# Performance work log

Measured on AMD Instinct MI355X. Metric: run time of the kernel, lower is better.

## Reference

```python
import jax, jax.numpy as jnp
import numpy as np

# arch config (matches init_kwargs)
T = 8
G = 16
D = 64
GG = G * G
THR = 0.5            # arch.object_threshold
Z_COS_MATCH_W = 5.0  # arch.z_cos_match_weight
ADJ_W = 1.0
PRES_W = 1.0
POOL_W = 1.0
OBJ_W = 10.0
FLOW_W = 1.0
FULL_OBJ = 200000.0  # arch.full_object_weight
FLOW_END = 100000.0  # arch.flow_cooling_end_step


def setup_inputs() -> dict:
    key = jax.random.key(0)
    k1, k2, k3 = jax.random.split(key, 3)
    B = 128
    return {
        "z_what": jax.random.normal(k1, (T * B, GG, D), dtype=jnp.float32),
        "z_pres_prob": jax.random.uniform(k2, (T * B, GG, 1), dtype=jnp.float32),
        "grid_flow": jax.random.uniform(k3, (T * B, GG, 1), dtype=jnp.float32),
        "global_step": 50000,
    }


def _maxpool3x3(x):
    # x: (N, C, G, G); torch MaxPool2d(3, stride=1, padding=1) pads with -inf
    return jax.lax.reduce_window(
        x, -jnp.inf, jax.lax.max,
        window_dimensions=(1, 1, 3, 3), window_strides=(1, 1, 1, 1),
        padding=[(0, 0), (0, 0), (1, 1), (1, 1)])


def reference(z_what, z_pres_prob, grid_flow, global_step):
    B = z_what.shape[0] // T
    zw = z_what.reshape(T, B, GG, D)
    zp = z_pres_prob.reshape(T, B, GG, 1)

    # ---- z_what_loss_grid_cell: adjacent squared deltas ----
    z_what_loss = jnp.sum((zw[1:] - zw[:-1]) ** 2)

    # ---- z_pres_loss_grid_cell ----
    sim = 1.0 - (zp[2:] - zp[:-2]) ** 2
    deltas = (zp[2:] - zp[1:-1]) ** 2 + (zp[:-2] - zp[1:-1]) ** 2
    z_pres_loss = jnp.sum(sim * deltas)

    # ---- z_what_consistency_pool (cosine_sim branch) ----
    w = jnp.abs(zw) * zp                                    # (T,B,GG,D)
    wi = w.transpose(0, 1, 3, 2).reshape(T * B, D, G, G)
    smoothed = _maxpool3x3(wi).reshape(T, B, D, GG).transpose(0, 1, 3, 2)
    dot = jnp.sum(smoothed[:-1] * w[1:], axis=-1)           # (T-1,B,GG)
    na = jnp.maximum(jnp.sqrt(jnp.sum(smoothed[:-1] ** 2, -1)), 1e-6)
    nb = jnp.maximum(jnp.sqrt(jnp.sum(w[1:] ** 2, -1)), 1e-6)
    cos_pool = dot / (na * nb)
    pw = zp[..., 0]
    pw = (pw[:-1] + pw[1:]) * 0.5                           # (T-1,B,GG)
    z_what_loss_pool = -jnp.sum(cos_pool * pw)

    # ---- z_what_consistency_objects (vectorized over objects) ----
    # For every active cell (t,b,i,j) at time t<T-1, compare its z_what (prior)
    # with z_what at t+1 over the 3x3 circular neighborhood, restricted to
    # neighbor cells whose z_pres > threshold. Loss per object:
    #   -z_cos_match_weight * max(sim) + sum(sim); skipped if no active neighbor.
    zpg = zp.reshape(T, B, G, G)
    zwg = zw.reshape(T, B, G, G, D)
    prior = zwg[:-1]                                        # (T-1,B,G,G,D)
    prior_n = jnp.maximum(jnp.sqrt(jnp.sum(prior ** 2, -1)), 1e-8)
    pres_prior = zpg[:-1] > THR                             # (T-1,B,G,G)
    sum_sim = jnp.zeros(prior.shape[:-1], dtype=prior.dtype)
    max_sim = jnp.full(prior.shape[:-1], -jnp.inf, dtype=prior.dtype)
    has_nb = jnp.zeros(prior.shape[:-1], dtype=bool)
    for di in (-1, 0, 1):
        for dj in (-1, 0, 1):
            nbw = jnp.roll(zwg[1:], (-di, -dj), axis=(2, 3))       # circular
            nbp = jnp.roll(zpg[1:], (-di, -dj), axis=(2, 3)) > THR
            dotn = jnp.sum(prior * nbw, axis=-1)
            nn = jnp.maximum(jnp.sqrt(jnp.sum(nbw ** 2, -1)), 1e-8)
            s = dotn / (prior_n * nn)
            sum_sim = sum_sim + jnp.where(nbp, s, 0.0)
            max_sim = jnp.maximum(max_sim, jnp.where(nbp, s, -jnp.inf))
            has_nb = has_nb | nbp
    valid = pres_prior & has_nb
    contrib = jnp.where(valid, -Z_COS_MATCH_W * max_sim + sum_sim, 0.0)
    z_what_loss_objects = jnp.sum(contrib)
    objects_detected = jnp.sum(pres_prior.astype(jnp.int32))

    # ---- compute_flow_loss ----
    zp_img = z_pres_prob.reshape(-1, 1, G, G)
    zp_max = _maxpool3x3(zp_img).reshape(-1, GG, 1)
    flow = grid_flow.reshape(-1, GG, 1)
    fmask = flow > 0.5
    flow_loss = jnp.sum(jnp.where(fmask, (zp_max - flow) ** 2, 0.0)) \
        + 100.0 * jnp.maximum(0.0, jnp.sum(zp_img) - jnp.sum(flow))

    # ---- total (Space base loss excluded; external submodule) ----
    scale_obj = min(1.0, float(global_step) / FULL_OBJ)
    scale_flow = max(0.0, 1.0 - float(global_step) / FLOW_END)
    loss = (z_what_loss * ADJ_W
            + z_pres_loss * PRES_W
            + z_what_loss_pool * POOL_W
            + z_what_loss_objects * scale_obj * OBJ_W
            + flow_loss * FLOW_W * scale_flow)
    return loss
```

## Files before the change

kernel.cpp:

```cpp
#include <hip/hip_runtime.h>
#include <math.h>

#define TT 8
#define BB 128
#define GG 256
#define DD 64
#define NCH 4
#define CF4 4
#define ST 5
#define NPAIR ((TT - 1) * BB)


__device__ inline float wred(float v) {
#pragma unroll
    for (int off = 32; off > 0; off >>= 1) v += __shfl_xor(v, off, 64);
    return v;
}
__device__ inline float dot4(float4 a, float4 b) {
    return a.x * b.x + a.y * b.y + a.z * b.z + a.w * b.w;
}
__device__ inline float4 fabs4(float4 a) {
    return make_float4(fabsf(a.x), fabsf(a.y), fabsf(a.z), fabsf(a.w));
}
__device__ inline float4 max4(float4 a, float4 b) {
    return make_float4(fmaxf(a.x, b.x), fmaxf(a.y, b.y), fmaxf(a.z, b.z), fmaxf(a.w, b.w));
}
__device__ inline float4 scale4(float4 a, float s) {
    return make_float4(a.x * s, a.y * s, a.z * s, a.w * s);
}
__device__ inline float4 sub4(float4 a, float4 b) {
    return make_float4(a.x - b.x, a.y - b.y, a.z - b.z, a.w - b.w);
}
__device__ inline float4 shfl4(float4 v, int src) {
    return make_float4(__shfl(v.x, src, 64), __shfl(v.y, src, 64),
                       __shfl(v.z, src, 64), __shfl(v.w, src, 64));
}

__global__ __launch_bounds__(256) void pair_kernel(const float* __restrict__ zw,
                                                   const float* __restrict__ zp,
                                                   const float* __restrict__ flow,
                                                   float* __restrict__ part) {
    const int pairIdx = blockIdx.x;
    const int t = pairIdx >> 7;
    const int b = pairIdx & (BB - 1);
    const int tid = threadIdx.x;
    const int gi = tid >> 4, gj = tid & 15;
    const int lane = tid & 63;

    __shared__ float4 shS[GG * ST];
    __shared__ float pA[GG], pB[GG], nB[GG];
    __shared__ float bred[8][4];

    const float4* gA = (const float4*)zw + (size_t)(t * BB + b) * 1024;
    const float4* gB = gA + (size_t)BB * 1024;

    const float pAc = zp[(size_t)(t * BB + b) * GG + tid];
    const float pBc = zp[(size_t)((t + 1) * BB + b) * GG + tid];
    pA[tid] = pAc;
    pB[tid] = pBc;

    int nbc[9];
    unsigned inbM = 0;
    {
        int m = 0;
#pragma unroll
        for (int di = -1; di <= 1; di++) {
#pragma unroll
            for (int dj = -1; dj <= 1; dj++) {
                nbc[m] = (((gi + di) & 15) << 4) | ((gj + dj) & 15);
                if (((unsigned)(gi + di) < 16u) && ((unsigned)(gj + dj) < 16u))
                    inbM |= (1u << m);
                m++;
            }
        }
    }
    __syncthreads();

    float zdiff = 0.f, sa = 0.f, sb = 0.f, poolDot = 0.f, poolN = 0.f;
    float dots[9] = {0.f, 0.f, 0.f, 0.f, 0.f, 0.f, 0.f, 0.f, 0.f};

#pragma unroll 1
    for (int c = 0; c < NCH; c++) {
        float4 aA[CF4], aB[CF4], rm[CF4];
#pragma unroll
        for (int q = 0; q < CF4; q++) {
            aA[q] = gA[tid * 16 + c * CF4 + q];
            aB[q] = gB[tid * 16 + c * CF4 + q];
        }
#pragma unroll
        for (int q = 0; q < CF4; q++) {
            float4 d = sub4(aB[q], aA[q]);
            zdiff += dot4(d, d);
            sa += dot4(aA[q], aA[q]);
            sb += dot4(aB[q], aB[q]);
            dots[4] += dot4(aA[q], aB[q]);
            float4 wa = scale4(fabs4(aA[q]), pAc);
            rm[q] = wa;
            float4 lft = shfl4(wa, lane - 1);
            if (gj > 0) rm[q] = max4(rm[q], lft);
            float4 rgt = shfl4(wa, lane + 1);
            if (gj < 15) rm[q] = max4(rm[q], rgt);
            shS[tid * ST + q] = aB[q];
        }
        __syncthreads();

#pragma unroll
        for (int k = 0; k < 9; k++) {
            if (k == 4) continue;
            int base = nbc[k] * ST;
#pragma unroll
            for (int q = 0; q < CF4; q++) dots[k] += dot4(aA[q], shS[base + q]);
        }
        __syncthreads();

#pragma unroll
        for (int q = 0; q < CF4; q++) shS[tid * ST + q] = rm[q];
        __syncthreads();

#pragma unroll
        for (int q = 0; q < CF4; q++) {
            float4 sm = rm[q];
            if (gi > 0) sm = max4(sm, shS[(tid - 16) * ST + q]);
            if (gi < 15) sm = max4(sm, shS[(tid + 16) * ST + q]);
            poolDot += dot4(sm, fabs4(aB[q]));
            poolN += dot4(sm, sm);
        }
        __syncthreads();
    }

    nB[tid] = sqrtf(sb);
    __syncthreads();

    float prior_n = fmaxf(sqrtf(sa), 1e-8f);
    float sum_sim = 0.f, max_sim = -1e30f;
    bool has = false;
#pragma unroll
    for (int k = 0; k < 9; k++) {
        float nn = fmaxf(nB[nbc[k]], 1e-8f);
        float s = dots[k] / (prior_n * nn);
        if (pB[nbc[k]] > 0.5f) {
            sum_sim += s;
            max_sim = fmaxf(max_sim, s);
            has = true;
        }
    }
    float obj = ((pAc > 0.5f) && has) ? (sum_sim - 5.0f * max_sim) : 0.f;

    float na_pool = fmaxf(sqrtf(poolN), 1e-6f);
    float nb_pool = fmaxf(pBc * sqrtf(sb), 1e-6f);
    float poolc = -(pBc * poolDot) / (na_pool * nb_pool) * 0.5f * (pAc + pBc);

    float mx = pAc;
#pragma unroll
    for (int k = 0; k < 9; k++)
        if (k != 4 && ((inbM >> k) & 1u)) mx = fmaxf(mx, pA[nbc[k]]);
    float f = flow[(size_t)(t * BB + b) * GG + tid];
    float fsq = 0.f;
    if (f > 0.5f) { float d = mx - f; fsq = d * d; }
    float szp = pAc, sflow = f;
    if (t == 6) {
        float mxB = pBc;
#pragma unroll
        for (int k = 0; k < 9; k++)
            if (k != 4 && ((inbM >> k) & 1u)) mxB = fmaxf(mxB, pB[nbc[k]]);
        float f7 = flow[(size_t)(7 * BB + b) * GG + tid];
        if (f7 > 0.5f) { float d = mxB - f7; fsq += d * d; }
        szp += pBc;
        sflow += f7;
    }

    float pres = 0.f;
    if (t <= 5) {
        float pC = zp[(size_t)((t + 2) * BB + b) * GG + tid];
        float s02 = pC - pAc;
        float sim = 1.f - s02 * s02;
        float d2 = pC - pBc, d0 = pAc - pBc;
        pres = sim * (d2 * d2 + d0 * d0);
    }

    float r[7] = {zdiff, pres, poolc, obj, fsq, szp, sflow};
    int w = tid >> 6;
#pragma unroll
    for (int j = 0; j < 7; j++) {
        float rv = wred(r[j]);
        if (lane == 0) bred[j][w] = rv;
    }
    __syncthreads();
    if (tid < 7)
        part[pairIdx * 8 + tid] = bred[tid][0] + bred[tid][1] + bred[tid][2] + bred[tid][3];
}

__global__ __launch_bounds__(256) void final_kernel(const float* __restrict__ part,
                                                    const int* __restrict__ gs,
                                                    float* __restrict__ out) {
    const int tid = threadIdx.x;
    __shared__ float bred[7][4];
    float c[7] = {0.f, 0.f, 0.f, 0.f, 0.f, 0.f, 0.f};
    for (int p = tid; p < NPAIR; p += 256) {
        const float* r = part + p * 8;
#pragma unroll
        for (int j = 0; j < 7; j++) c[j] += r[j];
    }
    int w = tid >> 6, lane = tid & 63;
#pragma unroll
    for (int j = 0; j < 7; j++) {
        float rv = wred(c[j]);
        if (lane == 0) bred[j][w] = rv;
    }
    __syncthreads();
    if (tid == 0) {
        float s[7];
#pragma unroll
        for (int j = 0; j < 7; j++) s[j] = bred[j][0] + bred[j][1] + bred[j][2] + bred[j][3];
        float step = (float)gs[0];
        float scale_obj = fminf(1.f, step / 200000.f);
        float scale_flow = fmaxf(0.f, 1.f - step / 100000.f);
        float flow_loss = s[4] + 100.f * fmaxf(0.f, s[5] - s[6]);
        out[0] = s[0]
               + s[1]
               + s[2]
               + s[3] * scale_obj * 10.0f
               + flow_loss * scale_flow;
    }
}

extern "C" void kernel_launch(void* const* d_in, const int* in_sizes, int n_in,
                              void* d_out, int out_size, void* d_ws, size_t ws_size,
                              hipStream_t stream) {
    const float* zw = (const float*)d_in[0];
    const float* zp = (const float*)d_in[1];
    const float* fl = (const float*)d_in[2];
    const int* gs = (const int*)d_in[3];
    float* ws = (float*)d_ws;

    pair_kernel<<<NPAIR, 256, 0, stream>>>(zw, zp, fl, ws);
    final_kernel<<<1, 256, 0, stream>>>(ws, gs, (float*)d_out);
}
```

Measured before the change: 132.2 us.

## Prefetch next z_what chunk in registers and merge shared-memory phases

```diff
diff --git a/kernel.cpp b/kernel.cpp
--- a/kernel.cpp
+++ b/kernel.cpp
@@ -47,7 +47,8 @@
     const int gi = tid >> 4, gj = tid & 15;
     const int lane = tid & 63;
 
-    __shared__ float4 shS[GG * ST];
+    __shared__ float4 shB[GG * ST];
+    __shared__ float4 shR[GG * ST];
     __shared__ float pA[GG], pB[GG], nB[GG];
     __shared__ float bred[8][4];
 
@@ -56,6 +57,10 @@
 
     const float pAc = zp[(size_t)(t * BB + b) * GG + tid];
     const float pBc = zp[(size_t)((t + 1) * BB + b) * GG + tid];
+    const float f = flow[(size_t)(t * BB + b) * GG + tid];
+    float f7 = 0.f, pC = 0.f;
+    if (t == 6) f7 = flow[(size_t)(7 * BB + b) * GG + tid];
+    if (t <= 5) pC = zp[(size_t)((t + 2) * BB + b) * GG + tid];
     pA[tid] = pAc;
     pB[tid] = pBc;
 
@@ -74,33 +79,43 @@
             }
         }
     }
-    __syncthreads();
 
     float zdiff = 0.f, sa = 0.f, sb = 0.f, poolDot = 0.f, poolN = 0.f;
     float dots[9] = {0.f, 0.f, 0.f, 0.f, 0.f, 0.f, 0.f, 0.f, 0.f};
 
+    float4 cA[CF4], cB[CF4];
+#pragma unroll
+    for (int q = 0; q < CF4; q++) {
+        cA[q] = gA[tid * 16 + q];
+        cB[q] = gB[tid * 16 + q];
+    }
+
 #pragma unroll 1
     for (int c = 0; c < NCH; c++) {
-        float4 aA[CF4], aB[CF4], rm[CF4];
+        float4 nA4[CF4], nB4[CF4];
+        if (c + 1 < NCH) {
+#pragma unroll
+            for (int q = 0; q < CF4; q++) {
+                nA4[q] = gA[tid * 16 + (c + 1) * CF4 + q];
+                nB4[q] = gB[tid * 16 + (c + 1) * CF4 + q];
+            }
+        }
+
 #pragma unroll
         for (int q = 0; q < CF4; q++) {
-            aA[q] = gA[tid * 16 + c * CF4 + q];
-            aB[q] = gB[tid * 16 + c * CF4 + q];
-        }
-#pragma unroll
-        for (int q = 0; q < CF4; q++) {
-            float4 d = sub4(aB[q], aA[q]);
+            float4 d = sub4(cB[q], cA[q]);
             zdiff += dot4(d, d);
-            sa += dot4(aA[q], aA[q]);
-            sb += dot4(aB[q], aB[q]);
-            dots[4] += dot4(aA[q], aB[q]);
-            float4 wa = scale4(fabs4(aA[q]), pAc);
-            rm[q] = wa;
+            sa += dot4(cA[q], cA[q]);
+            sb += dot4(cB[q], cB[q]);
+            dots[4] += dot4(cA[q], cB[q]);
+            float4 wa = scale4(fabs4(cA[q]), pAc);
+            float4 rm = wa;
             float4 lft = shfl4(wa, lane - 1);
-            if (gj > 0) rm[q] = max4(rm[q], lft);
+            if (gj > 0) rm = max4(rm, lft);
             float4 rgt = shfl4(wa, lane + 1);
-            if (gj < 15) rm[q] = max4(rm[q], rgt);
-            shS[tid * ST + q] = aB[q];
+            if (gj < 15) rm = max4(rm, rgt);
+            shB[tid * ST + q] = cB[q];
+            shR[tid * ST + q] = rm;
         }
         __syncthreads();
 
@@ -109,23 +124,22 @@
             if (k == 4) continue;
             int base = nbc[k] * ST;
 #pragma unroll
-            for (int q = 0; q < CF4; q++) dots[k] += dot4(aA[q], shS[base + q]);
+            for (int q = 0; q < CF4; q++) dots[k] += dot4(cA[q], shB[base + q]);
+        }
+#pragma unroll
+        for (int q = 0; q < CF4; q++) {
+            float4 sm = shR[tid * ST + q];
+            if (gi > 0) sm = max4(sm, shR[(tid - 16) * ST + q]);
+            if (gi < 15) sm = max4(sm, shR[(tid + 16) * ST + q]);
+            poolDot += dot4(sm, fabs4(cB[q]));
+            poolN += dot4(sm, sm);
         }
         __syncthreads();
 
-#pragma unroll
-        for (int q = 0; q < CF4; q++) shS[tid * ST + q] = rm[q];
-        __syncthreads();
-
-#pragma unroll
-        for (int q = 0; q < CF4; q++) {
-            float4 sm = rm[q];
-            if (gi > 0) sm = max4(sm, shS[(tid - 16) * ST + q]);
-            if (gi < 15) sm = max4(sm, shS[(tid + 16) * ST + q]);
-            poolDot += dot4(sm, fabs4(aB[q]));
-            poolN += dot4(sm, sm);
-        }
-        __syncthreads();
+        if (c + 1 < NCH) {
+#pragma unroll
+            for (int q = 0; q < CF4; q++) { cA[q] = nA4[q]; cB[q] = nB4[q]; }
+        }
     }
 
     nB[tid] = sqrtf(sb);
@@ -154,7 +168,6 @@
 #pragma unroll
     for (int k = 0; k < 9; k++)
         if (k != 4 && ((inbM >> k) & 1u)) mx = fmaxf(mx, pA[nbc[k]]);
-    float f = flow[(size_t)(t * BB + b) * GG + tid];
     float fsq = 0.f;
     if (f > 0.5f) { float d = mx - f; fsq = d * d; }
     float szp = pAc, sflow = f;
@@ -163,7 +176,6 @@
 #pragma unroll
         for (int k = 0; k < 9; k++)
             if (k != 4 && ((inbM >> k) & 1u)) mxB = fmaxf(mxB, pB[nbc[k]]);
-        float f7 = flow[(size_t)(7 * BB + b) * GG + tid];
         if (f7 > 0.5f) { float d = mxB - f7; fsq += d * d; }
         szp += pBc;
         sflow += f7;
@@ -171,7 +183,6 @@
 
     float pres = 0.f;
     if (t <= 5) {
-        float pC = zp[(size_t)((t + 2) * BB + b) * GG + tid];
         float s02 = pC - pAc;
         float sim = 1.f - s02 * s02;
         float d2 = pC - pBc, d0 = pAc - pBc;
```

Result: slower. 158.2 us (+19.6%).
